# Performance work log

Hardware: AMD Instinct MI355X
Metric: run time of the kernel (lower is better)

Reference implementation:

```python
import jax, jax.numpy as jnp
import numpy as np
import math

# Module hyperparameters (match init_kwargs)
B_CAPS = 16   # input capsule types
C_CAPS = 32   # output capsule types
KSZ = 3       # kernel size
STRIDE = 1
P = 4         # pose matrix is P x P
PSIZE = P * P
LAMBDA = 0.01 # EM routing inverse-temperature (argv[1])
EPS = 1e-6
LN_2PI = math.log(2.0 * math.pi)


def patching(x, K, stride):
    """(b,h,w,B,d) -> (b,oh,ow,K*K*B,d), im2col-style window gather."""
    b, h, w, Bc, d = x.shape
    oh = (h - K) // stride + 1
    idxs = np.array([[hi + k for k in range(K)] for hi in range(0, h - K + 1, stride)])  # (oh, K)
    x = x[:, idxs]                                  # (b, oh, K, w, Bc, d)
    x = x[:, :, :, idxs]                            # (b, oh, K, ow, K, Bc, d)
    x = jnp.transpose(x, (0, 1, 3, 2, 4, 5, 6))     # (b, oh, ow, K, K, Bc, d)
    return x.reshape(b, oh, oh, K * K * Bc, d), oh, oh


def em_routing(v, a_in, beta_u, beta_a, lam, iters):
    """EM routing (Hinton et al., Matrix Capsules with EM Routing).
    v: (b,h,w,N,C,psize) votes; a_in: (b,h,w,N,1) input activations.
    Returns mu (b,h,w,C,psize), a_out (b,h,w,C,1).
    """
    b, h, w, N, C, ps = v.shape
    # r: assignment of input capsule i to output capsule j, weighted by a_in
    r = jnp.full((b, h, w, N, C), 1.0 / C, dtype=v.dtype) * a_in  # (b,h,w,N,C)
    for it in range(iters):
        # ---- M step ----
        r_sum = r.sum(axis=3, keepdims=True)                   # (b,h,w,1,C)
        coeff = (r / (r_sum + EPS))[..., None]                 # (b,h,w,N,C,1)
        mu = jnp.sum(coeff * v, axis=3, keepdims=True)         # (b,h,w,1,C,ps)
        sigma_sq = jnp.sum(coeff * (v - mu) ** 2, axis=3, keepdims=True) + EPS
        # beta_u: (C,1) broadcasts over the psize axis
        cost_h = (beta_u + 0.5 * jnp.log(sigma_sq)) * r_sum[..., None]  # (b,h,w,1,C,ps)
        logit = lam * (beta_a - cost_h.sum(axis=5, keepdims=True))      # (b,h,w,1,C,1)
        a_out = jax.nn.sigmoid(logit)
        # ---- E step ----
        if it < iters - 1:
            ln_p = (-((v - mu) ** 2) / (2.0 * sigma_sq)
                    - 0.5 * jnp.log(sigma_sq) - 0.5 * LN_2PI)   # (b,h,w,N,C,ps)
            ln_ap = ln_p.sum(axis=5) + jnp.log(a_out[..., 0] + EPS)  # (b,h,w,N,C)
            r = jax.nn.softmax(ln_ap, axis=4) * a_in
    mu = mu.reshape(b, h, w, C, ps)
    a_out = a_out.reshape(b, h, w, C, 1)
    return mu, a_out


def setup_inputs() -> dict:
    key = jax.random.key(0)
    k1, k2, k3 = jax.random.split(key, 3)
    x = jax.random.normal(k1, (4, 16, 16, B_CAPS, PSIZE), dtype=jnp.float32)
    a = jax.random.uniform(k2, (4, 16, 16, B_CAPS, 1), dtype=jnp.float32)
    weight = jax.random.normal(k3, (1, 1, 1, KSZ * KSZ * B_CAPS, C_CAPS, P, P), dtype=jnp.float32)
    beta_u = jnp.zeros((C_CAPS, 1), dtype=jnp.float32)
    beta_a = jnp.zeros((C_CAPS, 1), dtype=jnp.float32)
    return {"x": x, "a": a, "weight": weight, "beta_u": beta_u, "beta_a": beta_a, "iters": 2}


def reference(x, a, weight, beta_u, beta_a, iters):
    b = x.shape[0]
    p_in, oh, ow = patching(x, KSZ, STRIDE)   # (b,oh,ow,K*K*B,psize)
    a_in, _, _ = patching(a, KSZ, STRIDE)     # (b,oh,ow,K*K*B,1)
    N = KSZ * KSZ * B_CAPS
    # voting: per-capsule pose matmul x(P,P) @ W(P,P) broadcast over C
    v = jnp.einsum('bhwnij,ncjk->bhwncik',
                   p_in.reshape(b, oh, ow, N, P, P),
                   weight.reshape(N, C_CAPS, P, P))
    v = v.reshape(b, oh, ow, N, C_CAPS, PSIZE)
    p_out, a_out = em_routing(v, a_in, beta_u, beta_a, LAMBDA, iters)
    return p_out, a_out
```

## Files before the change

kernel.cpp:

```cpp
#include <hip/hip_runtime.h>


namespace {

constexpr int OHW  = 14;
constexpr int NPOS = 4 * OHW * OHW;
constexpr int NN   = 144;
constexpr int CC   = 32;
constexpr float LAMB  = 0.01f;
constexpr float EPSF  = 1e-6f;
constexpr float LN2PI = 1.8378770664093453f;
constexpr int NSUB = 8;
constexpr int NCH  = NN / NSUB;
constexpr int RST  = 36;

template <int CTRL>
__device__ __forceinline__ float dpp_mov(float x) {
  union { float f; int i; } u, r;
  u.f = x;
  r.i = __builtin_amdgcn_update_dpp(0, u.i, CTRL, 0xF, 0xF, true);
  return r.f;
}

__device__ __forceinline__ float swz_xor16(float x) {
  union { float f; int i; } u, r;
  u.f = x;
  r.i = __builtin_amdgcn_ds_swizzle(u.i, 0x401F);
  return r.f;
}

__device__ __forceinline__ void mat44(const float4 pr[4], const float4 wr[4], float v[16]) {
  #pragma unroll
  for (int i = 0; i < 4; ++i) {
    v[4*i+0] = fmaf(pr[i].x, wr[0].x, fmaf(pr[i].y, wr[1].x, fmaf(pr[i].z, wr[2].x, pr[i].w * wr[3].x)));
    v[4*i+1] = fmaf(pr[i].x, wr[0].y, fmaf(pr[i].y, wr[1].y, fmaf(pr[i].z, wr[2].y, pr[i].w * wr[3].y)));
    v[4*i+2] = fmaf(pr[i].x, wr[0].z, fmaf(pr[i].y, wr[1].z, fmaf(pr[i].z, wr[2].z, pr[i].w * wr[3].z)));
    v[4*i+3] = fmaf(pr[i].x, wr[0].w, fmaf(pr[i].y, wr[1].w, fmaf(pr[i].z, wr[2].w, pr[i].w * wr[3].w)));
  }
}

__global__ __launch_bounds__(256)
void convcaps_em(const float* __restrict__ x,
                 const float* __restrict__ a,
                 const float* __restrict__ w,
                 const float* __restrict__ beta_u,
                 const float* __restrict__ beta_a,
                 const int*   __restrict__ iters_p,
                 float* __restrict__ out_mu,
                 float* __restrict__ out_a)
{
  __shared__ __align__(16) float sP[NN * 16];
  __shared__ float sA[NN];
  __shared__ __align__(16) float sRed[4][CC][RST];
  __shared__ __align__(16) float sStat[CC][RST];

  const int tid = threadIdx.x;
  const int pos = blockIdx.x;
  const int b   = pos / (OHW * OHW);
  const int rem = pos - b * (OHW * OHW);
  const int oi  = rem / OHW;
  const int oj  = rem - oi * OHW;

  int iters = iters_p[0];
  iters = (iters < 1) ? 1 : (iters > 16 ? 16 : iters);

  #pragma unroll
  for (int t = 0; t < 9; ++t) {
    const int kh = t / 3, kw = t % 3;
    sP[t * 256 + tid] = x[(((b * 16 + oi + kh) * 16) + (oj + kw)) * 256 + tid];
  }
  if (tid < NN) {
    const int kh = tid / 48, kw = (tid >> 4) % 3, bc = tid & 15;
    sA[tid] = a[(((b * 16 + oi + kh) * 16) + (oj + kw)) * 16 + bc];
  }
  __syncthreads();

  const int lane = tid & 63;
  const int wv   = tid >> 6;
  const int c    = lane & 31;
  const int half = lane >> 5;
  const int sub  = wv * 2 + half;
  const float bu16 = 16.0f * beta_u[c];
  const float ba   = beta_a[c];

  float mu[16], hi[16], hm[16];
  float kcp = 0.f, aout = 0.f;

  for (int it = 0; it < iters; ++it) {
    float T0 = 0.f, T1[16], T2[16];
    #pragma unroll
    for (int p = 0; p < 16; ++p) { T1[p] = 0.f; T2[p] = 0.f; }

    const float4* W0 = (const float4*)(w + sub * 512 + c * 16);
    float4 wr[4] = {W0[0], W0[1], W0[2], W0[3]};

    if (it == 0) {
      #pragma unroll 1
      for (int ch = 0; ch < NCH; ++ch) {
        const int n = sub + NSUB * ch;
        const float4* Pp = (const float4*)(sP + n * 16);
        const float4 pr[4] = {Pp[0], Pp[1], Pp[2], Pp[3]};
        float v[16];
        mat44(pr, wr, v);
        if (ch < NCH - 1) {
          const float4* Wn = (const float4*)(w + (n + NSUB) * 512 + c * 16);
          wr[0] = Wn[0]; wr[1] = Wn[1]; wr[2] = Wn[2]; wr[3] = Wn[3];
        }
        const float rn = sA[n];
        T0 += rn;
        #pragma unroll
        for (int p = 0; p < 16; ++p) {
          const float rv = rn * v[p];
          T1[p] += rv;
          T2[p] = fmaf(rv, v[p], T2[p]);
        }
      }
    } else {
      #pragma unroll 1
      for (int ch = 0; ch < NCH; ++ch) {
        const int n = sub + NSUB * ch;
        const float4* Pp = (const float4*)(sP + n * 16);
        const float4 pr[4] = {Pp[0], Pp[1], Pp[2], Pp[3]};
        float v[16];
        mat44(pr, wr, v);
        if (ch < NCH - 1) {
          const float4* Wn = (const float4*)(w + (n + NSUB) * 512 + c * 16);
          wr[0] = Wn[0]; wr[1] = Wn[1]; wr[2] = Wn[2]; wr[3] = Wn[3];
        }
        float s0 = 0.f, s1 = 0.f, s2 = 0.f, s3 = 0.f;
        #pragma unroll
        for (int p = 0; p < 4; ++p) {
          s0 = fmaf(fmaf(hi[p],      v[p],      hm[p]),      v[p],      s0);
          s1 = fmaf(fmaf(hi[p + 4],  v[p + 4],  hm[p + 4]),  v[p + 4],  s1);
          s2 = fmaf(fmaf(hi[p + 8],  v[p + 8],  hm[p + 8]),  v[p + 8],  s2);
          s3 = fmaf(fmaf(hi[p + 12], v[p + 12], hm[p + 12]), v[p + 12], s3);
        }
        const float xv = kcp - ((s0 + s1) + (s2 + s3));
        float m = xv;
        m = fmaxf(m, dpp_mov<0x128>(m));
        m = fmaxf(m, dpp_mov<0x124>(m));
        m = fmaxf(m, dpp_mov<0x122>(m));
        m = fmaxf(m, dpp_mov<0x121>(m));
        m = fmaxf(m, swz_xor16(m));
        const float e = __expf(xv - m);
        float z = e;
        z += dpp_mov<0x128>(z);
        z += dpp_mov<0x124>(z);
        z += dpp_mov<0x122>(z);
        z += dpp_mov<0x121>(z);
        z += swz_xor16(z);
        const float rn = sA[n] * e * __builtin_amdgcn_rcpf(z);
        T0 += rn;
        #pragma unroll
        for (int p = 0; p < 16; ++p) {
          const float rv = rn * v[p];
          T1[p] += rv;
          T2[p] = fmaf(rv, v[p], T2[p]);
        }
      }
    }

    T0 += __shfl_xor(T0, 32);
    #pragma unroll
    for (int p = 0; p < 16; ++p) {
      T1[p] += __shfl_xor(T1[p], 32);
      T2[p] += __shfl_xor(T2[p], 32);
    }

    if (half == 0) {
      float4* d = (float4*)(&sRed[wv][c][0]);
      d[0] = make_float4(T1[0],  T1[1],  T1[2],  T1[3]);
      d[1] = make_float4(T1[4],  T1[5],  T1[6],  T1[7]);
      d[2] = make_float4(T1[8],  T1[9],  T1[10], T1[11]);
      d[3] = make_float4(T1[12], T1[13], T1[14], T1[15]);
      d[4] = make_float4(T2[0],  T2[1],  T2[2],  T2[3]);
      d[5] = make_float4(T2[4],  T2[5],  T2[6],  T2[7]);
      d[6] = make_float4(T2[8],  T2[9],  T2[10], T2[11]);
      d[7] = make_float4(T2[12], T2[13], T2[14], T2[15]);
      sRed[wv][c][32] = T0;
    }
    __syncthreads();
    {
      const int c2 = tid & 31;
      const int s2 = tid >> 5;
      const float q0 = sRed[0][c2][s2]      + sRed[1][c2][s2]      + sRed[2][c2][s2]      + sRed[3][c2][s2];
      const float q1 = sRed[0][c2][s2 + 8]  + sRed[1][c2][s2 + 8]  + sRed[2][c2][s2 + 8]  + sRed[3][c2][s2 + 8];
      const float q2 = sRed[0][c2][s2 + 16] + sRed[1][c2][s2 + 16] + sRed[2][c2][s2 + 16] + sRed[3][c2][s2 + 16];
      const float q3 = sRed[0][c2][s2 + 24] + sRed[1][c2][s2 + 24] + sRed[2][c2][s2 + 24] + sRed[3][c2][s2 + 24];
      sStat[c2][s2]      = q0;
      sStat[c2][s2 + 8]  = q1;
      sStat[c2][s2 + 16] = q2;
      sStat[c2][s2 + 24] = q3;
      if (tid < 32)
        sStat[tid][32] = sRed[0][tid][32] + sRed[1][tid][32] + sRed[2][tid][32] + sRed[3][tid][32];
    }
    __syncthreads();

    const float4* R = (const float4*)(&sStat[c][0]);
    const float4 u1a = R[0], u1b = R[1], u1c = R[2], u1d = R[3];
    const float4 u2a = R[4], u2b = R[5], u2c = R[6], u2d = R[7];
    const float U0 = sStat[c][32];
    float U1[16] = {u1a.x,u1a.y,u1a.z,u1a.w, u1b.x,u1b.y,u1b.z,u1b.w,
                    u1c.x,u1c.y,u1c.z,u1c.w, u1d.x,u1d.y,u1d.z,u1d.w};
    float U2[16] = {u2a.x,u2a.y,u2a.z,u2a.w, u2b.x,u2b.y,u2b.z,u2b.w,
                    u2c.x,u2c.y,u2c.z,u2c.w, u2d.x,u2d.y,u2d.z,u2d.w};

    const float inv  = 1.0f / (U0 + ((it == 0) ? (CC * EPSF) : EPSF));
    const float rsum = (it == 0) ? U0 * (1.0f / CC) : U0;
    float logsum = 0.f;
    #pragma unroll
    for (int p = 0; p < 16; ++p) {
      const float m = U1[p] * inv;
      mu[p] = m;
      float sig = fmaf(m, fmaf(m, U0, -2.0f * U1[p]), U2[p]) * inv + EPSF;
      sig = fmaxf(sig, 1e-12f);
      logsum += __logf(sig);
      hi[p] = 0.5f / sig;
    }
    const float cost = rsum * (bu16 + 0.5f * logsum);
    aout = 1.0f / (1.0f + __expf(-LAMB * (ba - cost)));

    if (it < iters - 1) {
      float K = 0.f;
      #pragma unroll
      for (int p = 0; p < 16; ++p) {
        hm[p] = -2.0f * hi[p] * mu[p];
        K = fmaf(hi[p] * mu[p], mu[p], K);
      }
      kcp = __logf(aout + EPSF) - 0.5f * logsum - 8.0f * LN2PI - K;
    }
  }

  if (tid < 32) {
    float4* om = (float4*)(out_mu + (size_t)pos * 512 + c * 16);
    om[0] = make_float4(mu[0],  mu[1],  mu[2],  mu[3]);
    om[1] = make_float4(mu[4],  mu[5],  mu[6],  mu[7]);
    om[2] = make_float4(mu[8],  mu[9],  mu[10], mu[11]);
    om[3] = make_float4(mu[12], mu[13], mu[14], mu[15]);
    out_a[pos * CC + c] = aout;
  }
}

}

extern "C" void kernel_launch(void* const* d_in, const int* in_sizes, int n_in,
                              void* d_out, int out_size, void* d_ws, size_t ws_size,
                              hipStream_t stream) {
  const float* x  = (const float*)d_in[0];
  const float* a  = (const float*)d_in[1];
  const float* w  = (const float*)d_in[2];
  const float* bu = (const float*)d_in[3];
  const float* ba = (const float*)d_in[4];
  const int* iters = (const int*)d_in[5];

  float* out_mu = (float*)d_out;
  float* out_a  = out_mu + (size_t)NPOS * CC * 16;

  convcaps_em<<<NPOS, 256, 0, stream>>>(x, a, w, bu, ba, iters, out_mu, out_a);
}
```

Measured before the change: 114.9 us.

## Split pose components across half-waves and double block size to 512 threads

Each wave half now computes 8 of the 16 pose components for one input capsule instead of a whole capsule, and the block grows to 512 threads with 8 waves each owning one input sub-slice. Per-thread register arrays halve, which allows higher occupancy (launch bounds 512,6), while the E-step distance, logsum and K terms are combined across halves with a shuffle. In exchange it adds a cross-half shuffle in the inner loop, loads each weight matrix redundantly in both halves, and makes the shared-memory reduction buffer larger with more wave partials to sum.

```diff
diff --git a/kernel.cpp b/kernel.cpp
--- a/kernel.cpp
+++ b/kernel.cpp
@@ -29,9 +29,9 @@
   return r.f;
 }
 
-__device__ __forceinline__ void mat44(const float4 pr[4], const float4 wr[4], float v[16]) {
+__device__ __forceinline__ void mat44h(const float4 pr[2], const float4 wr[4], float v[8]) {
   #pragma unroll
-  for (int i = 0; i < 4; ++i) {
+  for (int i = 0; i < 2; ++i) {
     v[4*i+0] = fmaf(pr[i].x, wr[0].x, fmaf(pr[i].y, wr[1].x, fmaf(pr[i].z, wr[2].x, pr[i].w * wr[3].x)));
     v[4*i+1] = fmaf(pr[i].x, wr[0].y, fmaf(pr[i].y, wr[1].y, fmaf(pr[i].z, wr[2].y, pr[i].w * wr[3].y)));
     v[4*i+2] = fmaf(pr[i].x, wr[0].z, fmaf(pr[i].y, wr[1].z, fmaf(pr[i].z, wr[2].z, pr[i].w * wr[3].z)));
@@ -39,7 +39,12 @@
   }
 }
 
-__global__ __launch_bounds__(256)
+__device__ __forceinline__ void loadw(float4 wr[4], const float* __restrict__ w, int n, int c) {
+  const float4* W = (const float4*)(w + n * 512 + c * 16);
+  wr[0] = W[0]; wr[1] = W[1]; wr[2] = W[2]; wr[3] = W[3];
+}
+
+__global__ __launch_bounds__(512, 6)
 void convcaps_em(const float* __restrict__ x,
                  const float* __restrict__ a,
                  const float* __restrict__ w,
@@ -51,7 +56,7 @@
 {
   __shared__ __align__(16) float sP[NN * 16];
   __shared__ float sA[NN];
-  __shared__ __align__(16) float sRed[4][CC][RST];
+  __shared__ __align__(16) float sRed[NSUB][CC][RST];
   __shared__ __align__(16) float sStat[CC][RST];
 
   const int tid = threadIdx.x;
@@ -64,10 +69,10 @@
   int iters = iters_p[0];
   iters = (iters < 1) ? 1 : (iters > 16 ? 16 : iters);
 
-  #pragma unroll
-  for (int t = 0; t < 9; ++t) {
+  for (int i = tid; i < NN * 16; i += 512) {
+    const int t = i >> 8, r = i & 255;
     const int kh = t / 3, kw = t % 3;
-    sP[t * 256 + tid] = x[(((b * 16 + oi + kh) * 16) + (oj + kw)) * 256 + tid];
+    sP[i] = x[(((b * 16 + oi + kh) * 16) + (oj + kw)) * 256 + r];
   }
   if (tid < NN) {
     const int kh = tid / 48, kw = (tid >> 4) % 3, bc = tid & 15;
@@ -78,38 +83,35 @@
   const int lane = tid & 63;
   const int wv   = tid >> 6;
   const int c    = lane & 31;
-  const int half = lane >> 5;
-  const int sub  = wv * 2 + half;
+  const int ph   = lane >> 5;
+  const int sub  = wv;
   const float bu16 = 16.0f * beta_u[c];
   const float ba   = beta_a[c];
 
-  float mu[16], hi[16], hm[16];
+  float mu[8], hi[8], hm[8];
   float kcp = 0.f, aout = 0.f;
 
   for (int it = 0; it < iters; ++it) {
-    float T0 = 0.f, T1[16], T2[16];
+    float T0 = 0.f, T1[8], T2[8];
     #pragma unroll
-    for (int p = 0; p < 16; ++p) { T1[p] = 0.f; T2[p] = 0.f; }
-
-    const float4* W0 = (const float4*)(w + sub * 512 + c * 16);
-    float4 wr[4] = {W0[0], W0[1], W0[2], W0[3]};
+    for (int p = 0; p < 8; ++p) { T1[p] = 0.f; T2[p] = 0.f; }
+
+    float4 wr[4];
+    loadw(wr, w, sub, c);
 
     if (it == 0) {
       #pragma unroll 1
       for (int ch = 0; ch < NCH; ++ch) {
         const int n = sub + NSUB * ch;
-        const float4* Pp = (const float4*)(sP + n * 16);
-        const float4 pr[4] = {Pp[0], Pp[1], Pp[2], Pp[3]};
-        float v[16];
-        mat44(pr, wr, v);
-        if (ch < NCH - 1) {
-          const float4* Wn = (const float4*)(w + (n + NSUB) * 512 + c * 16);
-          wr[0] = Wn[0]; wr[1] = Wn[1]; wr[2] = Wn[2]; wr[3] = Wn[3];
-        }
+        const float4* Pp = (const float4*)(sP + n * 16 + ph * 8);
+        const float4 pr[2] = {Pp[0], Pp[1]};
+        float v[8];
+        mat44h(pr, wr, v);
+        if (ch < NCH - 1) loadw(wr, w, n + NSUB, c);
         const float rn = sA[n];
         T0 += rn;
         #pragma unroll
-        for (int p = 0; p < 16; ++p) {
+        for (int p = 0; p < 8; ++p) {
           const float rv = rn * v[p];
           T1[p] += rv;
           T2[p] = fmaf(rv, v[p], T2[p]);
@@ -119,23 +121,20 @@
       #pragma unroll 1
       for (int ch = 0; ch < NCH; ++ch) {
         const int n = sub + NSUB * ch;
-        const float4* Pp = (const float4*)(sP + n * 16);
-        const float4 pr[4] = {Pp[0], Pp[1], Pp[2], Pp[3]};
-        float v[16];
-        mat44(pr, wr, v);
-        if (ch < NCH - 1) {
-          const float4* Wn = (const float4*)(w + (n + NSUB) * 512 + c * 16);
-          wr[0] = Wn[0]; wr[1] = Wn[1]; wr[2] = Wn[2]; wr[3] = Wn[3];
+        const float4* Pp = (const float4*)(sP + n * 16 + ph * 8);
+        const float4 pr[2] = {Pp[0], Pp[1]};
+        float v[8];
+        mat44h(pr, wr, v);
+        if (ch < NCH - 1) loadw(wr, w, n + NSUB, c);
+        float s0 = 0.f, s1 = 0.f;
+        #pragma unroll
+        for (int p = 0; p < 4; ++p) {
+          s0 = fmaf(fmaf(hi[p],     v[p],     hm[p]),     v[p],     s0);
+          s1 = fmaf(fmaf(hi[p + 4], v[p + 4], hm[p + 4]), v[p + 4], s1);
         }
-        float s0 = 0.f, s1 = 0.f, s2 = 0.f, s3 = 0.f;
-        #pragma unroll
-        for (int p = 0; p < 4; ++p) {
-          s0 = fmaf(fmaf(hi[p],      v[p],      hm[p]),      v[p],      s0);
-          s1 = fmaf(fmaf(hi[p + 4],  v[p + 4],  hm[p + 4]),  v[p + 4],  s1);
-          s2 = fmaf(fmaf(hi[p + 8],  v[p + 8],  hm[p + 8]),  v[p + 8],  s2);
-          s3 = fmaf(fmaf(hi[p + 12], v[p + 12], hm[p + 12]), v[p + 12], s3);
-        }
-        const float xv = kcp - ((s0 + s1) + (s2 + s3));
+        float s = s0 + s1;
+        s += __shfl_xor(s, 32);
+        const float xv = kcp - s;
         float m = xv;
         m = fmaxf(m, dpp_mov<0x128>(m));
         m = fmaxf(m, dpp_mov<0x124>(m));
@@ -152,7 +151,7 @@
         const float rn = sA[n] * e * __builtin_amdgcn_rcpf(z);
         T0 += rn;
         #pragma unroll
-        for (int p = 0; p < 16; ++p) {
+        for (int p = 0; p < 8; ++p) {
           const float rv = rn * v[p];
           T1[p] += rv;
           T2[p] = fmaf(rv, v[p], T2[p]);
@@ -160,56 +159,49 @@
       }
     }
 
-    T0 += __shfl_xor(T0, 32);
-    #pragma unroll
-    for (int p = 0; p < 16; ++p) {
-      T1[p] += __shfl_xor(T1[p], 32);
-      T2[p] += __shfl_xor(T2[p], 32);
-    }
-
-    if (half == 0) {
-      float4* d = (float4*)(&sRed[wv][c][0]);
-      d[0] = make_float4(T1[0],  T1[1],  T1[2],  T1[3]);
-      d[1] = make_float4(T1[4],  T1[5],  T1[6],  T1[7]);
-      d[2] = make_float4(T1[8],  T1[9],  T1[10], T1[11]);
-      d[3] = make_float4(T1[12], T1[13], T1[14], T1[15]);
-      d[4] = make_float4(T2[0],  T2[1],  T2[2],  T2[3]);
-      d[5] = make_float4(T2[4],  T2[5],  T2[6],  T2[7]);
-      d[6] = make_float4(T2[8],  T2[9],  T2[10], T2[11]);
-      d[7] = make_float4(T2[12], T2[13], T2[14], T2[15]);
-      sRed[wv][c][32] = T0;
+    {
+      float4* d1 = (float4*)(&sRed[wv][c][ph * 8]);
+      d1[0] = make_float4(T1[0], T1[1], T1[2], T1[3]);
+      d1[1] = make_float4(T1[4], T1[5], T1[6], T1[7]);
+      float4* d2 = (float4*)(&sRed[wv][c][16 + ph * 8]);
+      d2[0] = make_float4(T2[0], T2[1], T2[2], T2[3]);
+      d2[1] = make_float4(T2[4], T2[5], T2[6], T2[7]);
+      if (ph == 0) sRed[wv][c][32] = T0;
     }
     __syncthreads();
     {
       const int c2 = tid & 31;
       const int s2 = tid >> 5;
-      const float q0 = sRed[0][c2][s2]      + sRed[1][c2][s2]      + sRed[2][c2][s2]      + sRed[3][c2][s2];
-      const float q1 = sRed[0][c2][s2 + 8]  + sRed[1][c2][s2 + 8]  + sRed[2][c2][s2 + 8]  + sRed[3][c2][s2 + 8];
-      const float q2 = sRed[0][c2][s2 + 16] + sRed[1][c2][s2 + 16] + sRed[2][c2][s2 + 16] + sRed[3][c2][s2 + 16];
-      const float q3 = sRed[0][c2][s2 + 24] + sRed[1][c2][s2 + 24] + sRed[2][c2][s2 + 24] + sRed[3][c2][s2 + 24];
+      float q0 = 0.f, q1 = 0.f;
+      #pragma unroll
+      for (int wq = 0; wq < NSUB; ++wq) {
+        q0 += sRed[wq][c2][s2];
+        q1 += sRed[wq][c2][s2 + 16];
+      }
       sStat[c2][s2]      = q0;
-      sStat[c2][s2 + 8]  = q1;
-      sStat[c2][s2 + 16] = q2;
-      sStat[c2][s2 + 24] = q3;
-      if (tid < 32)
-        sStat[tid][32] = sRed[0][tid][32] + sRed[1][tid][32] + sRed[2][tid][32] + sRed[3][tid][32];
+      sStat[c2][s2 + 16] = q1;
+      if (tid < 32) {
+        float q = 0.f;
+        #pragma unroll
+        for (int wq = 0; wq < NSUB; ++wq) q += sRed[wq][tid][32];
+        sStat[tid][32] = q;
+      }
     }
     __syncthreads();
 
-    const float4* R = (const float4*)(&sStat[c][0]);
-    const float4 u1a = R[0], u1b = R[1], u1c = R[2], u1d = R[3];
-    const float4 u2a = R[4], u2b = R[5], u2c = R[6], u2d = R[7];
+    const float4* R1 = (const float4*)(&sStat[c][ph * 8]);
+    const float4 u1a = R1[0], u1b = R1[1];
+    const float4* R2 = (const float4*)(&sStat[c][16 + ph * 8]);
+    const float4 u2a = R2[0], u2b = R2[1];
     const float U0 = sStat[c][32];
-    float U1[16] = {u1a.x,u1a.y,u1a.z,u1a.w, u1b.x,u1b.y,u1b.z,u1b.w,
-                    u1c.x,u1c.y,u1c.z,u1c.w, u1d.x,u1d.y,u1d.z,u1d.w};
-    float U2[16] = {u2a.x,u2a.y,u2a.z,u2a.w, u2b.x,u2b.y,u2b.z,u2b.w,
-                    u2c.x,u2c.y,u2c.z,u2c.w, u2d.x,u2d.y,u2d.z,u2d.w};
+    const float U1[8] = {u1a.x,u1a.y,u1a.z,u1a.w, u1b.x,u1b.y,u1b.z,u1b.w};
+    const float U2[8] = {u2a.x,u2a.y,u2a.z,u2a.w, u2b.x,u2b.y,u2b.z,u2b.w};
 
     const float inv  = 1.0f / (U0 + ((it == 0) ? (CC * EPSF) : EPSF));
     const float rsum = (it == 0) ? U0 * (1.0f / CC) : U0;
     float logsum = 0.f;
     #pragma unroll
-    for (int p = 0; p < 16; ++p) {
+    for (int p = 0; p < 8; ++p) {
       const float m = U1[p] * inv;
       mu[p] = m;
       float sig = fmaf(m, fmaf(m, U0, -2.0f * U1[p]), U2[p]) * inv + EPSF;
@@ -217,27 +209,27 @@
       logsum += __logf(sig);
       hi[p] = 0.5f / sig;
     }
+    logsum += __shfl_xor(logsum, 32);
     const float cost = rsum * (bu16 + 0.5f * logsum);
     aout = 1.0f / (1.0f + __expf(-LAMB * (ba - cost)));
 
     if (it < iters - 1) {
       float K = 0.f;
       #pragma unroll
-      for (int p = 0; p < 16; ++p) {
+      for (int p = 0; p < 8; ++p) {
         hm[p] = -2.0f * hi[p] * mu[p];
         K = fmaf(hi[p] * mu[p], mu[p], K);
       }
+      K += __shfl_xor(K, 32);
       kcp = __logf(aout + EPSF) - 0.5f * logsum - 8.0f * LN2PI - K;
     }
   }
 
-  if (tid < 32) {
-    float4* om = (float4*)(out_mu + (size_t)pos * 512 + c * 16);
-    om[0] = make_float4(mu[0],  mu[1],  mu[2],  mu[3]);
-    om[1] = make_float4(mu[4],  mu[5],  mu[6],  mu[7]);
-    om[2] = make_float4(mu[8],  mu[9],  mu[10], mu[11]);
-    om[3] = make_float4(mu[12], mu[13], mu[14], mu[15]);
-    out_a[pos * CC + c] = aout;
+  if (wv == 0) {
+    float4* om = (float4*)(out_mu + (size_t)pos * 512 + c * 16 + ph * 8);
+    om[0] = make_float4(mu[0], mu[1], mu[2], mu[3]);
+    om[1] = make_float4(mu[4], mu[5], mu[6], mu[7]);
+    if (ph == 0) out_a[pos * CC + c] = aout;
   }
 }
 
@@ -256,5 +248,5 @@
   float* out_mu = (float*)d_out;
   float* out_a  = out_mu + (size_t)NPOS * CC * 16;
 
-  convcaps_em<<<NPOS, 256, 0, stream>>>(x, a, w, bu, ba, iters, out_mu, out_a);
-}
+  convcaps_em<<<NPOS, 512, 0, stream>>>(x, a, w, bu, ba, iters, out_mu, out_a);
+}
```

Result: slower. 184.3 us (+60.4%).
